# Kernel tuning notes

Measured on AMD Instinct MI355X. Metric: run time of the kernel, lower is better.

## Reference

```python
import jax, jax.numpy as jnp
import numpy as np

B, DX, DZ, DY = 8192, 512, 1024, 256


def setup_inputs() -> dict:
    key = jax.random.key(0)
    ks = jax.random.split(key, 13)
    s = 0.02
    return {
        "xs": jax.random.normal(ks[0], (B, DX), dtype=jnp.float32),
        "Wx": jax.random.normal(ks[1], (DZ, DX), dtype=jnp.float32) * s,
        "bx": jnp.zeros((DZ,), dtype=jnp.float32),
        "Wy": jax.random.normal(ks[2], (DZ, DY), dtype=jnp.float32) * s,
        "by": jnp.zeros((DZ,), dtype=jnp.float32),
        "Wn": jax.random.normal(ks[3], (DZ, 3 * DZ), dtype=jnp.float32) * s,
        "bn": jnp.zeros((DZ,), dtype=jnp.float32),
        "Wu": jax.random.normal(ks[4], (DY, DZ), dtype=jnp.float32) * s,
        "bu": jnp.zeros((DY,), dtype=jnp.float32),
        "Wq": jax.random.normal(ks[5], (DY, DZ), dtype=jnp.float32) * s,
        "bq": jnp.zeros((DY,), dtype=jnp.float32),
        "ys_init": jax.random.normal(ks[6], (B, DY), dtype=jnp.float32),
        "zs_init": jax.random.normal(ks[7], (B, DZ), dtype=jnp.float32),
        "T": 4,
        "n": 6,
    }


def reference(xs, Wx, bx, Wy, by, Wn, bn, Wu, bu, Wq, bq, ys_init, zs_init, T, n):
    xs_e = xs @ Wx.T + bx                      # [B, DZ]
    ys_e = ys_init @ Wy.T + by                 # [B, DZ]
    zs = zs_init                               # [B, DZ]
    null = jnp.zeros_like(xs_e)

    def query(x, y, z):
        w = jnp.concatenate([x, y, z], axis=-1)  # [B, 3*DZ]
        return jnp.tanh(w @ Wn.T + bn)

    # no-grad refinement (T-1 outer iterations)
    for _ in range(T - 1):
        for _ in range(n):
            zs = query(xs_e, ys_e, zs)
        ys_e = query(null, ys_e, zs)
    ys_e = jax.lax.stop_gradient(ys_e)
    zs = jax.lax.stop_gradient(zs)

    # final grad-enabled block
    for _ in range(n):
        zs = query(xs_e, ys_e, zs)
    ys_e = query(null, ys_e, zs)

    y_hat = jax.nn.sigmoid(ys_e @ Wu.T + bu)
    q_hat = jax.nn.sigmoid(ys_e @ Wq.T + bq)
    return (y_hat, q_hat)
```

## Files before the change

### kernel.cpp

```cpp
#include <hip/hip_runtime.h>
#include <hip/hip_bf16.h>
#include <cstdint>
#include <cstddef>

#define B_   8192
#define DX_  512
#define DZ_  1024
#define DY_  256
#define T_   4
#define NN_  6

typedef float f32x4 __attribute__((ext_vector_type(4)));
typedef short s16x8 __attribute__((ext_vector_type(8)));
typedef __hip_bfloat16 bf16;

__device__ __forceinline__ void gload_lds16(const bf16* g, void* l) {
  __builtin_amdgcn_global_load_lds(
      (const __attribute__((address_space(1))) void*)g,
      (__attribute__((address_space(3))) void*)l,
      16, 0, 0);
}

__device__ __forceinline__ float bf2f(unsigned short u) {
  union { unsigned int i; float f; } cv; cv.i = ((unsigned int)u) << 16; return cv.f;
}

__global__ void cvt_bf16_kernel(const float* __restrict__ in, bf16* __restrict__ out, int n4) {
  int i = blockIdx.x * blockDim.x + threadIdx.x;
  if (i >= n4) return;
  float4 v = ((const float4*)in)[i];
  ushort4 o;
  bf16 a0 = __float2bfloat16(v.x); o.x = *(unsigned short*)&a0;
  bf16 a1 = __float2bfloat16(v.y); o.y = *(unsigned short*)&a1;
  bf16 a2 = __float2bfloat16(v.z); o.z = *(unsigned short*)&a2;
  bf16 a3 = __float2bfloat16(v.w); o.w = *(unsigned short*)&a3;
  ((ushort4*)out)[i] = o;
}

__global__ void pack_bias_kernel(const float* __restrict__ a, const float* __restrict__ b,
                                 float* __restrict__ o) {
  int i = threadIdx.x;
  o[i] = (i < DY_) ? a[i] : b[i - DY_];
}

template<int ACT, int MODE, bool HASADD>
__global__ __launch_bounds__(512, 2)
void gemm_bt(const bf16* __restrict__ A, int lda,
             const bf16* __restrict__ W, int ldw,
             const float* __restrict__ bias,
             const bf16* __restrict__ add1,
             bf16* __restrict__ out_pre,
             void* __restrict__ out, void* __restrict__ out2,
             int N, int K)
{
  __shared__ __align__(16) char ldsc[3 * 49152];
  const int t    = threadIdx.x;
  const int lane = t & 63;
  const int wave = t >> 6;
  const int m0 = blockIdx.x * 256;
  const int n0 = blockIdx.y * 128;

  const int srow = t >> 3;
  const int q    = (t & 7) ^ ((t >> 3) & 7);
  const bf16* gA = A + (size_t)(m0 + srow) * lda + q * 8;
  const bf16* gB = W + (size_t)(n0 + srow) * ldw + q * 8;
  const int wb = wave * 1024;

  auto stage = [&](int kt) {
    char* base = ldsc + (kt % 3) * 49152;
    const int ko = kt << 6;
#pragma unroll
    for (int i = 0; i < 4; ++i)
      gload_lds16(gA + (size_t)(i * 64) * lda + ko, base + i * 8192 + wb);
#pragma unroll
    for (int i = 0; i < 2; ++i)
      gload_lds16(gB + (size_t)(i * 64) * ldw + ko, base + 32768 + i * 8192 + wb);
  };

  const int mo = (wave >> 1) * 64;
  const int no = (wave & 1) * 64;
  const int fr = lane & 15;
  const int g4 = lane >> 4;
  const int rb = g4 * 4;

  const int NT = K >> 6;

  float bv[4] = {0.f, 0.f, 0.f, 0.f};
  if (bias) {
#pragma unroll
    for (int j = 0; j < 4; ++j) bv[j] = bias[n0 + no + j * 16 + fr];
  }
  unsigned short adr[4][4][4];
  if (HASADD && MODE != 1) {
#pragma unroll
    for (int f = 0; f < 4; ++f)
#pragma unroll
      for (int j = 0; j < 4; ++j) {
        const unsigned short* p = (const unsigned short*)add1
            + (size_t)(m0 + mo + f * 16 + rb) * N + (n0 + no + j * 16 + fr);
#pragma unroll
        for (int r = 0; r < 4; ++r) adr[f][j][r] = p[(size_t)r * N];
      }
  }
  __builtin_amdgcn_sched_barrier(0);
  stage(0);
  stage(1);
  __builtin_amdgcn_sched_barrier(0);

  f32x4 acc[4][4];
#pragma unroll
  for (int f = 0; f < 4; ++f)
#pragma unroll
    for (int j = 0; j < 4; ++j)
#pragma unroll
      for (int r = 0; r < 4; ++r) {
        float v = bv[j];
        if (HASADD && MODE != 1) v += bf2f(adr[f][j][r]);
        acc[f][j][r] = v;
      }

  s16x8 a0[4], b0[4], a1[4], b1[4];
  auto ldfrags = [&](int kt, int s, s16x8* fa, s16x8* fb) {
    const char* pA = ldsc + (kt % 3) * 49152;
    const char* pB = pA + 32768;
    const int cb = ((s * 4 + g4) ^ (fr & 7)) * 16;
#pragma unroll
    for (int f = 0; f < 4; ++f) fa[f] = *(const s16x8*)(pA + (mo + f * 16 + fr) * 128 + cb);
#pragma unroll
    for (int j = 0; j < 4; ++j) fb[j] = *(const s16x8*)(pB + (no + j * 16 + fr) * 128 + cb);
  };
  auto domfma = [&](const s16x8* fa, const s16x8* fb) {
    __builtin_amdgcn_s_setprio(1);
#pragma unroll
    for (int f = 0; f < 4; ++f)
#pragma unroll
      for (int j = 0; j < 4; ++j)
        acc[f][j] = __builtin_amdgcn_mfma_f32_16x16x32_bf16(fa[f], fb[j], acc[f][j], 0, 0, 0);
    __builtin_amdgcn_s_setprio(0);
  };

  asm volatile("s_waitcnt vmcnt(6)" ::: "memory");
  __builtin_amdgcn_s_barrier();

  for (int kt = 0; kt < NT; ++kt) {
    ldfrags(kt, 0, a0, b0);
    __builtin_amdgcn_sched_barrier(0);
    __builtin_amdgcn_s_barrier();
    asm volatile("s_waitcnt lgkmcnt(0)" ::: "memory");
    __builtin_amdgcn_sched_barrier(0);
    domfma(a0, b0);
    ldfrags(kt, 1, a1, b1);
    if (kt + 2 < NT) stage(kt + 2);
    __builtin_amdgcn_sched_barrier(0);
    if (kt + 2 < NT) asm volatile("s_waitcnt vmcnt(6)" ::: "memory");
    else             asm volatile("s_waitcnt vmcnt(0)" ::: "memory");
    __builtin_amdgcn_s_barrier();
    asm volatile("s_waitcnt lgkmcnt(0)" ::: "memory");
    __builtin_amdgcn_sched_barrier(0);
    domfma(a1, b1);
  }

#pragma unroll
  for (int f = 0; f < 4; ++f) {
#pragma unroll
    for (int j = 0; j < 4; ++j) {
      const int n = n0 + no + j * 16 + fr;
#pragma unroll
      for (int r = 0; r < 4; ++r) {
        const int m = m0 + mo + f * 16 + rb + r;
        float v = acc[f][j][r];
        if (MODE == 1) {
          out_pre[(size_t)m * N + n] = __float2bfloat16(v);
          v += bf2f(((const unsigned short*)add1)[(size_t)m * N + n]);
        }
        if (ACT == 1)      { float e = __expf(2.f * v); v = 1.f - 2.f / (e + 1.f); }
        else if (ACT == 2) v = 1.f / (1.f + __expf(-v));
        if (MODE == 2) {
          if (n < DY_) ((float*)out)[(size_t)m * DY_ + n] = v;
          else         ((float*)out2)[(size_t)m * DY_ + (n - DY_)] = v;
        } else {
          ((bf16*)out)[(size_t)m * N + n] = __float2bfloat16(v);
        }
      }
    }
  }
}

extern "C" void kernel_launch(void* const* d_in, const int* in_sizes, int n_in,
                              void* d_out, int out_size, void* d_ws, size_t ws_size,
                              hipStream_t stream) {
  const float* xs  = (const float*)d_in[0];
  const float* Wx  = (const float*)d_in[1];
  const float* bx  = (const float*)d_in[2];
  const float* Wy  = (const float*)d_in[3];
  const float* by  = (const float*)d_in[4];
  const float* Wn  = (const float*)d_in[5];
  const float* bn  = (const float*)d_in[6];
  const float* Wu  = (const float*)d_in[7];
  const float* bu  = (const float*)d_in[8];
  const float* Wq  = (const float*)d_in[9];
  const float* bq  = (const float*)d_in[10];
  const float* ys0 = (const float*)d_in[11];
  const float* zs0 = (const float*)d_in[12];

  char* ws = (char*)d_ws;
  size_t off = 0;
  auto take = [&](size_t bytes) -> char* {
    char* p = ws + off;
    off += (bytes + 255) & ~(size_t)255;
    return p;
  };

  bf16*  Wn_b  = (bf16*)take((size_t)DZ_ * 3 * DZ_ * 2);
  bf16*  Wx_b  = (bf16*)take((size_t)DZ_ * DX_ * 2);
  bf16*  Wy_b  = (bf16*)take((size_t)DZ_ * DY_ * 2);
  bf16*  Wuq_b = (bf16*)take((size_t)2 * DY_ * DZ_ * 2);
  float* buq   = (float*)take((size_t)2 * DY_ * 4);
  bf16*  ys_b  = (bf16*)take((size_t)B_ * DZ_ * 2);
  bf16*  z_a   = (bf16*)take((size_t)B_ * DZ_ * 2);
  bf16*  z_b   = (bf16*)take((size_t)B_ * DZ_ * 2);
  bf16*  cx    = (bf16*)take((size_t)B_ * DZ_ * 2);
  bf16*  cy    = (bf16*)take((size_t)B_ * DZ_ * 2);
  bf16*  c     = (bf16*)take((size_t)B_ * DZ_ * 2);
  bf16* xs_b   = c;
  bf16* ysin_b = (bf16*)((char*)c + (size_t)B_ * DX_ * 2);
  bf16* xse_b  = cy;

  auto cvt = [&](const float* src, bf16* dst, size_t n) {
    int n4 = (int)(n / 4);
    cvt_bf16_kernel<<<(n4 + 255) / 256, 256, 0, stream>>>(src, dst, n4);
  };
  cvt(Wn, Wn_b, (size_t)DZ_ * 3 * DZ_);
  cvt(Wx, Wx_b, (size_t)DZ_ * DX_);
  cvt(Wy, Wy_b, (size_t)DZ_ * DY_);
  cvt(Wu, Wuq_b, (size_t)DY_ * DZ_);
  cvt(Wq, Wuq_b + (size_t)DY_ * DZ_, (size_t)DY_ * DZ_);
  cvt(xs, xs_b, (size_t)B_ * DX_);
  cvt(ys0, ysin_b, (size_t)B_ * DY_);
  cvt(zs0, z_a, (size_t)B_ * DZ_);
  pack_bias_kernel<<<1, 512, 0, stream>>>(bu, bq, buq);

  const dim3 blk(512);
  const dim3 gz(B_ / 256, DZ_ / 128);
  const dim3 gh(B_ / 256, 4);

  gemm_bt<0, 0, false><<<gz, blk, 0, stream>>>(xs_b, DX_, Wx_b, DX_, bx, nullptr, nullptr, xse_b, nullptr, DZ_, DX_);
  gemm_bt<0, 0, false><<<gz, blk, 0, stream>>>(ysin_b, DY_, Wy_b, DY_, by, nullptr, nullptr, ys_b, nullptr, DZ_, DY_);
  gemm_bt<0, 0, false><<<gz, blk, 0, stream>>>(xse_b, DZ_, Wn_b, 3 * DZ_, nullptr, nullptr, nullptr, cx, nullptr, DZ_, DZ_);

  bf16* zc = z_a;
  bf16* zn = z_b;
  for (int tt = 0; tt < T_; ++tt) {
    gemm_bt<0, 1, true><<<gz, blk, 0, stream>>>(ys_b, DZ_, Wn_b + DZ_, 3 * DZ_, bn, cx, cy, c, nullptr, DZ_, DZ_);
    for (int i = 0; i < NN_; ++i) {
      gemm_bt<1, 0, true><<<gz, blk, 0, stream>>>(zc, DZ_, Wn_b + 2 * DZ_, 3 * DZ_, nullptr, c, nullptr, zn, nullptr, DZ_, DZ_);
      bf16* tmp = zc; zc = zn; zn = tmp;
    }
    gemm_bt<1, 0, true><<<gz, blk, 0, stream>>>(zc, DZ_, Wn_b + 2 * DZ_, 3 * DZ_, nullptr, cy, nullptr, ys_b, nullptr, DZ_, DZ_);
  }

  float* outp = (float*)d_out;
  gemm_bt<2, 2, false><<<gh, blk, 0, stream>>>(ys_b, DZ_, Wuq_b, DZ_, buq, nullptr, nullptr,
                                               outp, outp + (size_t)B_ * DY_, 2 * DY_, DZ_);
}
```

Baseline: 941.8 us.

## Fuse recurrent GEMM chain into persistent kernel with per-band flag sync

Replaces the roughly 30 separate recurrent GEMM launches with a single persistent kernel on a 32x8 grid. Each row band of 256 rows synchronises only with its own 8 column blocks through atomic counters, so different bands can run ahead of each other instead of waiting at global kernel boundaries. The x- and y-projection partial products (cx, cy) are held as packed bf16 in registers rather than written to and re-read from global memory. The kernel relies on all 256 blocks being resident at once, since a block that is not scheduled would deadlock the spin-waits, and it runs at one block per CU.

```diff
diff --git a/kernel.cpp b/kernel.cpp
--- a/kernel.cpp
+++ b/kernel.cpp
@@ -23,6 +23,16 @@
 
 __device__ __forceinline__ float bf2f(unsigned short u) {
   union { unsigned int i; float f; } cv; cv.i = ((unsigned int)u) << 16; return cv.f;
+}
+__device__ __forceinline__ float lo2f(unsigned int p) {
+  union { unsigned int i; float f; } cv; cv.i = p << 16; return cv.f;
+}
+__device__ __forceinline__ float hi2f(unsigned int p) {
+  union { unsigned int i; float f; } cv; cv.i = p & 0xffff0000u; return cv.f;
+}
+__device__ __forceinline__ unsigned int pk2(float a, float b) {
+  bf16 x = __float2bfloat16(a), y = __float2bfloat16(b);
+  return (unsigned int)*(unsigned short*)&x | ((unsigned int)*(unsigned short*)&y << 16);
 }
 
 __global__ void cvt_bf16_kernel(const float* __restrict__ in, bf16* __restrict__ out, int n4) {
@@ -43,15 +53,209 @@
   o[i] = (i < DY_) ? a[i] : b[i - DY_];
 }
 
-template<int ACT, int MODE, bool HASADD>
+__device__ __forceinline__ void band_arrive(unsigned int* flags, int idx) {
+  __syncthreads();
+  if (threadIdx.x == 0)
+    __hip_atomic_fetch_add(&flags[idx], 1u, __ATOMIC_RELEASE, __HIP_MEMORY_SCOPE_AGENT);
+}
+__device__ __forceinline__ void band_wait(unsigned int* flags, int idx) {
+  if (threadIdx.x == 0) {
+    while (__hip_atomic_load(&flags[idx], __ATOMIC_RELAXED, __HIP_MEMORY_SCOPE_AGENT) < 8u)
+      __builtin_amdgcn_s_sleep(2);
+  }
+  __syncthreads();
+  if ((threadIdx.x & 63) == 0)
+    (void)__hip_atomic_load(&flags[idx], __ATOMIC_ACQUIRE, __HIP_MEMORY_SCOPE_AGENT);
+}
+
+__global__ __launch_bounds__(512, 1)
+void trm_persist(const bf16* __restrict__ xs_b, const bf16* __restrict__ ysin_b,
+                 bf16* __restrict__ z_a, bf16* __restrict__ z_b,
+                 const bf16* __restrict__ Wx_b, const bf16* __restrict__ Wy_b,
+                 const bf16* __restrict__ Wn_b,
+                 const float* __restrict__ bx, const float* __restrict__ by,
+                 const float* __restrict__ bn,
+                 bf16* __restrict__ xse, bf16* __restrict__ ys,
+                 unsigned int* __restrict__ flags)
+{
+  __shared__ __align__(16) char ldsc[3 * 49152];
+  const int t    = threadIdx.x;
+  const int lane = t & 63;
+  const int wave = t >> 6;
+  const int band = blockIdx.x;
+  const int m0 = band * 256;
+  const int n0 = blockIdx.y * 128;
+
+  const int srow = t >> 3;
+  const int q    = (t & 7) ^ ((t >> 3) & 7);
+  const int wb   = wave * 1024;
+
+  const int mo = (wave >> 1) * 64;
+  const int no = (wave & 1) * 64;
+  const int fr = lane & 15;
+  const int g4 = lane >> 4;
+  const int rb = g4 * 4;
+
+  f32x4 acc[4][4];
+  unsigned int cx_pk[4][4][2], cy_pk[4][4][2];
+  s16x8 fa[4], fb[4];
+
+  auto core = [&](const bf16* A, int lda, const bf16* W, int ldw, int NT) {
+    const bf16* gA = A + (size_t)(m0 + srow) * lda + q * 8;
+    const bf16* gB = W + (size_t)(n0 + srow) * ldw + q * 8;
+    auto stage = [&](int kt) {
+      char* base = ldsc + (kt % 3) * 49152;
+      const int ko = kt << 6;
+#pragma unroll
+      for (int i = 0; i < 4; ++i)
+        gload_lds16(gA + (size_t)(i * 64) * lda + ko, base + i * 8192 + wb);
+#pragma unroll
+      for (int i = 0; i < 2; ++i)
+        gload_lds16(gB + (size_t)(i * 64) * ldw + ko, base + 32768 + i * 8192 + wb);
+    };
+    auto ldfrags = [&](int kt, int s) {
+      const char* pA = ldsc + (kt % 3) * 49152;
+      const char* pB = pA + 32768;
+      const int cb = ((s * 4 + g4) ^ (fr & 7)) * 16;
+#pragma unroll
+      for (int f = 0; f < 4; ++f) fa[f] = *(const s16x8*)(pA + (mo + f * 16 + fr) * 128 + cb);
+#pragma unroll
+      for (int j = 0; j < 4; ++j) fb[j] = *(const s16x8*)(pB + (no + j * 16 + fr) * 128 + cb);
+    };
+    auto domfma = [&]() {
+      __builtin_amdgcn_s_setprio(1);
+#pragma unroll
+      for (int f = 0; f < 4; ++f)
+#pragma unroll
+        for (int j = 0; j < 4; ++j)
+          acc[f][j] = __builtin_amdgcn_mfma_f32_16x16x32_bf16(fa[f], fb[j], acc[f][j], 0, 0, 0);
+      __builtin_amdgcn_s_setprio(0);
+    };
+
+    stage(0); stage(1);
+    asm volatile("s_waitcnt vmcnt(6)" ::: "memory");
+    __builtin_amdgcn_s_barrier();
+    for (int kt = 0; kt < NT; ++kt) {
+      ldfrags(kt, 0);
+      __builtin_amdgcn_sched_barrier(0);
+      __builtin_amdgcn_s_barrier();
+      asm volatile("s_waitcnt lgkmcnt(0)" ::: "memory");
+      __builtin_amdgcn_sched_barrier(0);
+      domfma();
+      ldfrags(kt, 1);
+      if (kt + 2 < NT) stage(kt + 2);
+      __builtin_amdgcn_sched_barrier(0);
+      if (kt + 2 < NT) asm volatile("s_waitcnt vmcnt(6)" ::: "memory");
+      else             asm volatile("s_waitcnt vmcnt(0)" ::: "memory");
+      __builtin_amdgcn_s_barrier();
+      asm volatile("s_waitcnt lgkmcnt(0)" ::: "memory");
+      __builtin_amdgcn_sched_barrier(0);
+      domfma();
+    }
+  };
+
+  auto initbias = [&](const float* bias) {
+    float bv[4];
+#pragma unroll
+    for (int j = 0; j < 4; ++j) bv[j] = bias ? bias[n0 + no + j * 16 + fr] : 0.f;
+#pragma unroll
+    for (int f = 0; f < 4; ++f)
+#pragma unroll
+      for (int j = 0; j < 4; ++j)
+#pragma unroll
+        for (int r = 0; r < 4; ++r) acc[f][j][r] = bv[j];
+  };
+  auto store_out = [&](bf16* o, int dotanh) {
+#pragma unroll
+    for (int f = 0; f < 4; ++f)
+#pragma unroll
+      for (int j = 0; j < 4; ++j) {
+        const int n = n0 + no + j * 16 + fr;
+#pragma unroll
+        for (int r = 0; r < 4; ++r) {
+          const int m = m0 + mo + f * 16 + rb + r;
+          float v = acc[f][j][r];
+          if (dotanh) { float e = __expf(2.f * v); v = 1.f - 2.f / (e + 1.f); }
+          o[(size_t)m * DZ_ + n] = __float2bfloat16(v);
+        }
+      }
+  };
+
+  initbias(bx);
+  core(xs_b, DX_, Wx_b, DX_, DX_ / 64);
+  store_out(xse, 0);
+  band_arrive(flags, 0 * 32 + band);
+
+  initbias(by);
+  core(ysin_b, DY_, Wy_b, DY_, DY_ / 64);
+  store_out(ys, 0);
+  band_arrive(flags, 1 * 32 + band);
+
+  band_wait(flags, 0 * 32 + band);
+  initbias(nullptr);
+  core(xse, DZ_, Wn_b, 3 * DZ_, DZ_ / 64);
+#pragma unroll
+  for (int f = 0; f < 4; ++f)
+#pragma unroll
+    for (int j = 0; j < 4; ++j) {
+      cx_pk[f][j][0] = pk2(acc[f][j][0], acc[f][j][1]);
+      cx_pk[f][j][1] = pk2(acc[f][j][2], acc[f][j][3]);
+    }
+
+  int ysflag = 1, zf = 2, zprev = -1;
+  bf16* zc = z_a;
+  bf16* zn = z_b;
+  for (int tt = 0; tt < T_; ++tt) {
+    band_wait(flags, ysflag * 32 + band);
+    initbias(bn);
+    core(ys, DZ_, Wn_b + DZ_, 3 * DZ_, DZ_ / 64);
+#pragma unroll
+    for (int f = 0; f < 4; ++f)
+#pragma unroll
+      for (int j = 0; j < 4; ++j) {
+        cy_pk[f][j][0] = pk2(acc[f][j][0], acc[f][j][1]);
+        cy_pk[f][j][1] = pk2(acc[f][j][2], acc[f][j][3]);
+      }
+    for (int i = 0; i < NN_; ++i) {
+      if (zprev >= 0) band_wait(flags, zprev * 32 + band);
+      else            __syncthreads();
+#pragma unroll
+      for (int f = 0; f < 4; ++f)
+#pragma unroll
+        for (int j = 0; j < 4; ++j) {
+          acc[f][j][0] = lo2f(cy_pk[f][j][0]) + lo2f(cx_pk[f][j][0]);
+          acc[f][j][1] = hi2f(cy_pk[f][j][0]) + hi2f(cx_pk[f][j][0]);
+          acc[f][j][2] = lo2f(cy_pk[f][j][1]) + lo2f(cx_pk[f][j][1]);
+          acc[f][j][3] = hi2f(cy_pk[f][j][1]) + hi2f(cx_pk[f][j][1]);
+        }
+      core(zc, DZ_, Wn_b + 2 * DZ_, 3 * DZ_, DZ_ / 64);
+      store_out(zn, 1);
+      band_arrive(flags, zf * 32 + band);
+      zprev = zf; ++zf;
+      bf16* tmp = zc; zc = zn; zn = tmp;
+    }
+    band_wait(flags, zprev * 32 + band);
+#pragma unroll
+    for (int f = 0; f < 4; ++f)
+#pragma unroll
+      for (int j = 0; j < 4; ++j) {
+        acc[f][j][0] = lo2f(cy_pk[f][j][0]);
+        acc[f][j][1] = hi2f(cy_pk[f][j][0]);
+        acc[f][j][2] = lo2f(cy_pk[f][j][1]);
+        acc[f][j][3] = hi2f(cy_pk[f][j][1]);
+      }
+    core(zc, DZ_, Wn_b + 2 * DZ_, 3 * DZ_, DZ_ / 64);
+    store_out(ys, 1);
+    band_arrive(flags, zf * 32 + band);
+    ysflag = zf; ++zf;
+  }
+}
+
 __global__ __launch_bounds__(512, 2)
-void gemm_bt(const bf16* __restrict__ A, int lda,
-             const bf16* __restrict__ W, int ldw,
-             const float* __restrict__ bias,
-             const bf16* __restrict__ add1,
-             bf16* __restrict__ out_pre,
-             void* __restrict__ out, void* __restrict__ out2,
-             int N, int K)
+void head_gemm(const bf16* __restrict__ A,
+               const bf16* __restrict__ W,
+               const float* __restrict__ bias,
+               float* __restrict__ out, float* __restrict__ out2)
 {
   __shared__ __align__(16) char ldsc[3 * 49152];
   const int t    = threadIdx.x;
@@ -59,6 +263,7 @@
   const int wave = t >> 6;
   const int m0 = blockIdx.x * 256;
   const int n0 = blockIdx.y * 128;
+  const int N = 2 * DY_, K = DZ_, lda = DZ_, ldw = DZ_;
 
   const int srow = t >> 3;
   const int q    = (t & 7) ^ ((t >> 3) & 7);
@@ -83,44 +288,19 @@
   const int g4 = lane >> 4;
   const int rb = g4 * 4;
 
-  const int NT = K >> 6;
-
-  float bv[4] = {0.f, 0.f, 0.f, 0.f};
-  if (bias) {
-#pragma unroll
-    for (int j = 0; j < 4; ++j) bv[j] = bias[n0 + no + j * 16 + fr];
-  }
-  unsigned short adr[4][4][4];
-  if (HASADD && MODE != 1) {
-#pragma unroll
-    for (int f = 0; f < 4; ++f)
-#pragma unroll
-      for (int j = 0; j < 4; ++j) {
-        const unsigned short* p = (const unsigned short*)add1
-            + (size_t)(m0 + mo + f * 16 + rb) * N + (n0 + no + j * 16 + fr);
-#pragma unroll
-        for (int r = 0; r < 4; ++r) adr[f][j][r] = p[(size_t)r * N];
-      }
-  }
-  __builtin_amdgcn_sched_barrier(0);
-  stage(0);
-  stage(1);
-  __builtin_amdgcn_sched_barrier(0);
-
+  float bv[4];
+#pragma unroll
+  for (int j = 0; j < 4; ++j) bv[j] = bias[n0 + no + j * 16 + fr];
   f32x4 acc[4][4];
 #pragma unroll
   for (int f = 0; f < 4; ++f)
 #pragma unroll
     for (int j = 0; j < 4; ++j)
 #pragma unroll
-      for (int r = 0; r < 4; ++r) {
-        float v = bv[j];
-        if (HASADD && MODE != 1) v += bf2f(adr[f][j][r]);
-        acc[f][j][r] = v;
-      }
-
-  s16x8 a0[4], b0[4], a1[4], b1[4];
-  auto ldfrags = [&](int kt, int s, s16x8* fa, s16x8* fb) {
+      for (int r = 0; r < 4; ++r) acc[f][j][r] = bv[j];
+
+  s16x8 fa[4], fb[4];
+  auto ldfrags = [&](int kt, int s) {
     const char* pA = ldsc + (kt % 3) * 49152;
     const char* pB = pA + 32768;
     const int cb = ((s * 4 + g4) ^ (fr & 7)) * 16;
@@ -129,7 +309,7 @@
 #pragma unroll
     for (int j = 0; j < 4; ++j) fb[j] = *(const s16x8*)(pB + (no + j * 16 + fr) * 128 + cb);
   };
-  auto domfma = [&](const s16x8* fa, const s16x8* fb) {
+  auto domfma = [&]() {
     __builtin_amdgcn_s_setprio(1);
 #pragma unroll
     for (int f = 0; f < 4; ++f)
@@ -139,17 +319,18 @@
     __builtin_amdgcn_s_setprio(0);
   };
 
+  const int NT = K >> 6;
+  stage(0); stage(1);
   asm volatile("s_waitcnt vmcnt(6)" ::: "memory");
   __builtin_amdgcn_s_barrier();
-
   for (int kt = 0; kt < NT; ++kt) {
-    ldfrags(kt, 0, a0, b0);
+    ldfrags(kt, 0);
     __builtin_amdgcn_sched_barrier(0);
     __builtin_amdgcn_s_barrier();
     asm volatile("s_waitcnt lgkmcnt(0)" ::: "memory");
     __builtin_amdgcn_sched_barrier(0);
-    domfma(a0, b0);
-    ldfrags(kt, 1, a1, b1);
+    domfma();
+    ldfrags(kt, 1);
     if (kt + 2 < NT) stage(kt + 2);
     __builtin_amdgcn_sched_barrier(0);
     if (kt + 2 < NT) asm volatile("s_waitcnt vmcnt(6)" ::: "memory");
@@ -157,11 +338,11 @@
     __builtin_amdgcn_s_barrier();
     asm volatile("s_waitcnt lgkmcnt(0)" ::: "memory");
     __builtin_amdgcn_sched_barrier(0);
-    domfma(a1, b1);
+    domfma();
   }
 
 #pragma unroll
-  for (int f = 0; f < 4; ++f) {
+  for (int f = 0; f < 4; ++f)
 #pragma unroll
     for (int j = 0; j < 4; ++j) {
       const int n = n0 + no + j * 16 + fr;
@@ -169,21 +350,11 @@
       for (int r = 0; r < 4; ++r) {
         const int m = m0 + mo + f * 16 + rb + r;
         float v = acc[f][j][r];
-        if (MODE == 1) {
-          out_pre[(size_t)m * N + n] = __float2bfloat16(v);
-          v += bf2f(((const unsigned short*)add1)[(size_t)m * N + n]);
-        }
-        if (ACT == 1)      { float e = __expf(2.f * v); v = 1.f - 2.f / (e + 1.f); }
-        else if (ACT == 2) v = 1.f / (1.f + __expf(-v));
-        if (MODE == 2) {
-          if (n < DY_) ((float*)out)[(size_t)m * DY_ + n] = v;
-          else         ((float*)out2)[(size_t)m * DY_ + (n - DY_)] = v;
-        } else {
-          ((bf16*)out)[(size_t)m * N + n] = __float2bfloat16(v);
-        }
+        v = 1.f / (1.f + __expf(-v));
+        if (n < DY_) out[(size_t)m * DY_ + n] = v;
+        else         out2[(size_t)m * DY_ + (n - DY_)] = v;
       }
     }
-  }
 }
 
 extern "C" void kernel_launch(void* const* d_in, const int* in_sizes, int n_in,
@@ -211,20 +382,18 @@
     return p;
   };
 
-  bf16*  Wn_b  = (bf16*)take((size_t)DZ_ * 3 * DZ_ * 2);
-  bf16*  Wx_b  = (bf16*)take((size_t)DZ_ * DX_ * 2);
-  bf16*  Wy_b  = (bf16*)take((size_t)DZ_ * DY_ * 2);
-  bf16*  Wuq_b = (bf16*)take((size_t)2 * DY_ * DZ_ * 2);
-  float* buq   = (float*)take((size_t)2 * DY_ * 4);
-  bf16*  ys_b  = (bf16*)take((size_t)B_ * DZ_ * 2);
-  bf16*  z_a   = (bf16*)take((size_t)B_ * DZ_ * 2);
-  bf16*  z_b   = (bf16*)take((size_t)B_ * DZ_ * 2);
-  bf16*  cx    = (bf16*)take((size_t)B_ * DZ_ * 2);
-  bf16*  cy    = (bf16*)take((size_t)B_ * DZ_ * 2);
-  bf16*  c     = (bf16*)take((size_t)B_ * DZ_ * 2);
-  bf16* xs_b   = c;
-  bf16* ysin_b = (bf16*)((char*)c + (size_t)B_ * DX_ * 2);
-  bf16* xse_b  = cy;
+  bf16*  Wn_b   = (bf16*)take((size_t)DZ_ * 3 * DZ_ * 2);
+  bf16*  Wx_b   = (bf16*)take((size_t)DZ_ * DX_ * 2);
+  bf16*  Wy_b   = (bf16*)take((size_t)DZ_ * DY_ * 2);
+  bf16*  Wuq_b  = (bf16*)take((size_t)2 * DY_ * DZ_ * 2);
+  float* buq    = (float*)take((size_t)2 * DY_ * 4);
+  bf16*  ys_b   = (bf16*)take((size_t)B_ * DZ_ * 2);
+  bf16*  z_a    = (bf16*)take((size_t)B_ * DZ_ * 2);
+  bf16*  z_b    = (bf16*)take((size_t)B_ * DZ_ * 2);
+  bf16*  xse_b  = (bf16*)take((size_t)B_ * DZ_ * 2);
+  bf16*  xs_b   = (bf16*)take((size_t)B_ * DX_ * 2);
+  bf16*  ysin_b = (bf16*)take((size_t)B_ * DY_ * 2);
+  unsigned int* flags = (unsigned int*)take(32 * 32 * 4);
 
   auto cvt = [&](const float* src, bf16* dst, size_t n) {
     int n4 = (int)(n / 4);
@@ -239,27 +408,12 @@
   cvt(ys0, ysin_b, (size_t)B_ * DY_);
   cvt(zs0, z_a, (size_t)B_ * DZ_);
   pack_bias_kernel<<<1, 512, 0, stream>>>(bu, bq, buq);
-
-  const dim3 blk(512);
-  const dim3 gz(B_ / 256, DZ_ / 128);
-  const dim3 gh(B_ / 256, 4);
-
-  gemm_bt<0, 0, false><<<gz, blk, 0, stream>>>(xs_b, DX_, Wx_b, DX_, bx, nullptr, nullptr, xse_b, nullptr, DZ_, DX_);
-  gemm_bt<0, 0, false><<<gz, blk, 0, stream>>>(ysin_b, DY_, Wy_b, DY_, by, nullptr, nullptr, ys_b, nullptr, DZ_, DY_);
-  gemm_bt<0, 0, false><<<gz, blk, 0, stream>>>(xse_b, DZ_, Wn_b, 3 * DZ_, nullptr, nullptr, nullptr, cx, nullptr, DZ_, DZ_);
-
-  bf16* zc = z_a;
-  bf16* zn = z_b;
-  for (int tt = 0; tt < T_; ++tt) {
-    gemm_bt<0, 1, true><<<gz, blk, 0, stream>>>(ys_b, DZ_, Wn_b + DZ_, 3 * DZ_, bn, cx, cy, c, nullptr, DZ_, DZ_);
-    for (int i = 0; i < NN_; ++i) {
-      gemm_bt<1, 0, true><<<gz, blk, 0, stream>>>(zc, DZ_, Wn_b + 2 * DZ_, 3 * DZ_, nullptr, c, nullptr, zn, nullptr, DZ_, DZ_);
-      bf16* tmp = zc; zc = zn; zn = tmp;
-    }
-    gemm_bt<1, 0, true><<<gz, blk, 0, stream>>>(zc, DZ_, Wn_b + 2 * DZ_, 3 * DZ_, nullptr, cy, nullptr, ys_b, nullptr, DZ_, DZ_);
-  }
+  hipMemsetAsync(flags, 0, 32 * 32 * 4, stream);
+
+  trm_persist<<<dim3(32, 8), 512, 0, stream>>>(
+      xs_b, ysin_b, z_a, z_b, Wx_b, Wy_b, Wn_b, bx, by, bn, xse_b, ys_b, flags);
 
   float* outp = (float*)d_out;
-  gemm_bt<2, 2, false><<<gh, blk, 0, stream>>>(ys_b, DZ_, Wuq_b, DZ_, buq, nullptr, nullptr,
-                                               outp, outp + (size_t)B_ * DY_, 2 * DY_, DZ_);
-}
+  head_gemm<<<dim3(32, 4), 512, 0, stream>>>(ys_b, Wuq_b, buq,
+                                             outp, outp + (size_t)B_ * DY_);
+}
```

Measured after the change: 1.643 ms. 74.4% more time.

## Fuse conversion kernels and restructure GEMM k-loop to one barrier per iteration

Applied to the files above, without the earlier changes.

Nine separate fp32-to-bf16 conversion and bias-pack launches are merged into one grid-stride kernel, cutting launch overhead. The GEMM main loop is reordered: both LDS fragment halves are loaded up front, the first MFMA batch runs after a partial lgkmcnt wait, and the second after a full wait. The global-load wait and workgroup barrier move to the end of each iteration, so there is one barrier per k-tile instead of two. This risks LDS hazards if the triple-buffer staging does not cover the reordered reads, and holding both fragment sets at once raises register pressure.

```diff
diff --git a/kernel.cpp b/kernel.cpp
--- a/kernel.cpp
+++ b/kernel.cpp
@@ -25,22 +25,46 @@
   union { unsigned int i; float f; } cv; cv.i = ((unsigned int)u) << 16; return cv.f;
 }
 
-__global__ void cvt_bf16_kernel(const float* __restrict__ in, bf16* __restrict__ out, int n4) {
-  int i = blockIdx.x * blockDim.x + threadIdx.x;
-  if (i >= n4) return;
-  float4 v = ((const float4*)in)[i];
+__device__ __forceinline__ void cv4(const float* __restrict__ s, bf16* __restrict__ d, long i) {
+  float4 v = ((const float4*)s)[i];
   ushort4 o;
   bf16 a0 = __float2bfloat16(v.x); o.x = *(unsigned short*)&a0;
   bf16 a1 = __float2bfloat16(v.y); o.y = *(unsigned short*)&a1;
   bf16 a2 = __float2bfloat16(v.z); o.z = *(unsigned short*)&a2;
   bf16 a3 = __float2bfloat16(v.w); o.w = *(unsigned short*)&a3;
-  ((ushort4*)out)[i] = o;
-}
-
-__global__ void pack_bias_kernel(const float* __restrict__ a, const float* __restrict__ b,
-                                 float* __restrict__ o) {
-  int i = threadIdx.x;
-  o[i] = (i < DY_) ? a[i] : b[i - DY_];
+  ((ushort4*)d)[i] = o;
+}
+
+__global__ void cvt_all_kernel(const float* __restrict__ Wn, const float* __restrict__ Wx,
+                               const float* __restrict__ Wy, const float* __restrict__ Wu,
+                               const float* __restrict__ Wq, const float* __restrict__ xs,
+                               const float* __restrict__ ys0, const float* __restrict__ zs0,
+                               const float* __restrict__ bu, const float* __restrict__ bq,
+                               bf16* __restrict__ Wn_b, bf16* __restrict__ Wx_b,
+                               bf16* __restrict__ Wy_b, bf16* __restrict__ Wuq_b,
+                               bf16* __restrict__ xs_b, bf16* __restrict__ ysin_b,
+                               bf16* __restrict__ z_a, float* __restrict__ buq) {
+  const long NWN = (long)DZ_ * 3 * DZ_ / 4, NWX = (long)DZ_ * DX_ / 4,
+             NWY = (long)DZ_ * DY_ / 4,     NWU = (long)DY_ * DZ_ / 4,
+             NXS = (long)B_ * DX_ / 4,      NYS = (long)B_ * DY_ / 4,
+             NZS = (long)B_ * DZ_ / 4,      NBQ = 2 * DY_ / 4;
+  const long total = NWN + NWX + NWY + 2 * NWU + NXS + NYS + NZS + NBQ;
+  for (long i = (long)blockIdx.x * blockDim.x + threadIdx.x; i < total;
+       i += (long)gridDim.x * blockDim.x) {
+    long j = i;
+    if (j < NWN) { cv4(Wn, Wn_b, j); continue; } j -= NWN;
+    if (j < NWX) { cv4(Wx, Wx_b, j); continue; } j -= NWX;
+    if (j < NWY) { cv4(Wy, Wy_b, j); continue; } j -= NWY;
+    if (j < NWU) { cv4(Wu, Wuq_b, j); continue; } j -= NWU;
+    if (j < NWU) { cv4(Wq, Wuq_b + (size_t)DY_ * DZ_ / 4 * 4, j); continue; } j -= NWU;
+    if (j < NXS) { cv4(xs, xs_b, j); continue; } j -= NXS;
+    if (j < NYS) { cv4(ys0, ysin_b, j); continue; } j -= NYS;
+    if (j < NZS) { cv4(zs0, z_a, j); continue; } j -= NZS;
+    float4 v;
+    if (j < DY_ / 4) v = ((const float4*)bu)[j];
+    else             v = ((const float4*)bq)[j - DY_ / 4];
+    ((float4*)buq)[j] = v;
+  }
 }
 
 template<int ACT, int MODE, bool HASADD>
@@ -141,23 +165,25 @@
 
   asm volatile("s_waitcnt vmcnt(6)" ::: "memory");
   __builtin_amdgcn_s_barrier();
+  __builtin_amdgcn_sched_barrier(0);
 
   for (int kt = 0; kt < NT; ++kt) {
     ldfrags(kt, 0, a0, b0);
-    __builtin_amdgcn_sched_barrier(0);
-    __builtin_amdgcn_s_barrier();
-    asm volatile("s_waitcnt lgkmcnt(0)" ::: "memory");
-    __builtin_amdgcn_sched_barrier(0);
-    domfma(a0, b0);
     ldfrags(kt, 1, a1, b1);
     if (kt + 2 < NT) stage(kt + 2);
     __builtin_amdgcn_sched_barrier(0);
-    if (kt + 2 < NT) asm volatile("s_waitcnt vmcnt(6)" ::: "memory");
-    else             asm volatile("s_waitcnt vmcnt(0)" ::: "memory");
-    __builtin_amdgcn_s_barrier();
+    asm volatile("s_waitcnt lgkmcnt(8)" ::: "memory");
+    __builtin_amdgcn_sched_barrier(0);
+    domfma(a0, b0);
     asm volatile("s_waitcnt lgkmcnt(0)" ::: "memory");
     __builtin_amdgcn_sched_barrier(0);
     domfma(a1, b1);
+    if (kt + 2 < NT)      asm volatile("s_waitcnt vmcnt(6)" ::: "memory");
+    else if (kt + 1 < NT) asm volatile("s_waitcnt vmcnt(0)" ::: "memory");
+    if (kt + 1 < NT) {
+      __builtin_amdgcn_s_barrier();
+      __builtin_amdgcn_sched_barrier(0);
+    }
   }
 
 #pragma unroll
@@ -211,34 +237,24 @@
     return p;
   };
 
-  bf16*  Wn_b  = (bf16*)take((size_t)DZ_ * 3 * DZ_ * 2);
-  bf16*  Wx_b  = (bf16*)take((size_t)DZ_ * DX_ * 2);
-  bf16*  Wy_b  = (bf16*)take((size_t)DZ_ * DY_ * 2);
-  bf16*  Wuq_b = (bf16*)take((size_t)2 * DY_ * DZ_ * 2);
-  float* buq   = (float*)take((size_t)2 * DY_ * 4);
-  bf16*  ys_b  = (bf16*)take((size_t)B_ * DZ_ * 2);
-  bf16*  z_a   = (bf16*)take((size_t)B_ * DZ_ * 2);
-  bf16*  z_b   = (bf16*)take((size_t)B_ * DZ_ * 2);
-  bf16*  cx    = (bf16*)take((size_t)B_ * DZ_ * 2);
-  bf16*  cy    = (bf16*)take((size_t)B_ * DZ_ * 2);
-  bf16*  c     = (bf16*)take((size_t)B_ * DZ_ * 2);
+  bf16*  Wn_b   = (bf16*)take((size_t)DZ_ * 3 * DZ_ * 2);
+  bf16*  Wx_b   = (bf16*)take((size_t)DZ_ * DX_ * 2);
+  bf16*  Wy_b   = (bf16*)take((size_t)DZ_ * DY_ * 2);
+  bf16*  Wuq_b  = (bf16*)take((size_t)2 * DY_ * DZ_ * 2);
+  float* buq    = (float*)take((size_t)2 * DY_ * 4);
+  bf16*  ys_b   = (bf16*)take((size_t)B_ * DZ_ * 2);
+  bf16*  z_a    = (bf16*)take((size_t)B_ * DZ_ * 2);
+  bf16*  z_b    = (bf16*)take((size_t)B_ * DZ_ * 2);
+  bf16*  cx     = (bf16*)take((size_t)B_ * DZ_ * 2);
+  bf16*  cy     = (bf16*)take((size_t)B_ * DZ_ * 2);
+  bf16*  c      = (bf16*)take((size_t)B_ * DZ_ * 2);
   bf16* xs_b   = c;
   bf16* ysin_b = (bf16*)((char*)c + (size_t)B_ * DX_ * 2);
   bf16* xse_b  = cy;
 
-  auto cvt = [&](const float* src, bf16* dst, size_t n) {
-    int n4 = (int)(n / 4);
-    cvt_bf16_kernel<<<(n4 + 255) / 256, 256, 0, stream>>>(src, dst, n4);
-  };
-  cvt(Wn, Wn_b, (size_t)DZ_ * 3 * DZ_);
-  cvt(Wx, Wx_b, (size_t)DZ_ * DX_);
-  cvt(Wy, Wy_b, (size_t)DZ_ * DY_);
-  cvt(Wu, Wuq_b, (size_t)DY_ * DZ_);
-  cvt(Wq, Wuq_b + (size_t)DY_ * DZ_, (size_t)DY_ * DZ_);
-  cvt(xs, xs_b, (size_t)B_ * DX_);
-  cvt(ys0, ysin_b, (size_t)B_ * DY_);
-  cvt(zs0, z_a, (size_t)B_ * DZ_);
-  pack_bias_kernel<<<1, 512, 0, stream>>>(bu, bq, buq);
+  cvt_all_kernel<<<2048, 256, 0, stream>>>(Wn, Wx, Wy, Wu, Wq, xs, ys0, zs0, bu, bq,
+                                           Wn_b, Wx_b, Wy_b, Wuq_b,
+                                           xs_b, ysin_b, z_a, buq);
 
   const dim3 blk(512);
   const dim3 gz(B_ / 256, DZ_ / 128);
```

Result: no change. 924.6 us (-1.8%).
